# Optimization experiments

Measured on AMD Instinct MI355X. Metric: run time of the kernel, lower is better.

The kernel has to match this reference:

```python
import jax, jax.numpy as jnp
import numpy as np

NUM_CLASSES = 81
NEG_RATIO = 3
POS_FRAC = 0.03  # realistic fraction of positive (matched) anchors


def setup_inputs() -> dict:
    key = jax.random.key(0)
    k1, k2, k3, k4, k5 = jax.random.split(key, 5)
    B, A, C = 64, 8732, NUM_CLASSES
    pred_loc = jax.random.normal(k1, (B, A, 4), dtype=jnp.float32)
    pred_conf = jax.random.normal(k2, (B, A, C), dtype=jnp.float32)
    gt_loc = jax.random.normal(k3, (B, A, 4), dtype=jnp.float32)
    raw_cls = jax.random.randint(k4, (B, A), 1, C)
    is_pos = jax.random.uniform(k5, (B, A)) < POS_FRAC
    gt_label = jnp.where(is_pos, raw_cls, 0).astype(jnp.int32)
    return {"pred_loc": pred_loc, "pred_conf": pred_conf, "gt_loc": gt_loc, "gt_label": gt_label}


def reference(pred_loc, pred_conf, gt_loc, gt_label):
    # pred_loc/gt_loc: [B, A, 4]; pred_conf: [B, A, C]; gt_label: [B, A] int
    pos = gt_label > 0  # [B, A]

    # Smooth L1 (beta=1), summed over positive anchors only (mask instead of boolean gather)
    d = jnp.abs(pred_loc - gt_loc)
    sl1 = jnp.where(d < 1.0, 0.5 * d * d, d - 0.5)
    loc_loss = jnp.sum(sl1 * pos[..., None].astype(sl1.dtype))

    # Per-anchor cross-entropy
    logp = jax.nn.log_softmax(pred_conf, axis=-1)  # [B, A, C]
    ce = -jnp.take_along_axis(logp, gt_label[..., None].astype(jnp.int32), axis=-1)[..., 0]  # [B, A]

    cef = ce.reshape(-1)
    posf = pos.reshape(-1)
    num_pos = jnp.sum(posf)
    num_neg = jnp.minimum(NEG_RATIO * num_pos, posf.size - num_pos)

    # Hard-negative mining: rank negatives by CE descending; select top num_neg.
    neg_vals = jnp.where(posf, -jnp.inf, cef)
    order = jnp.argsort(-neg_vals)  # indices sorted by descending negative loss
    rank = jnp.zeros_like(order).at[order].set(jnp.arange(order.size))
    neg_sel = (rank < num_neg) & (~posf)

    pos_conf_loss = jnp.sum(jnp.where(posf, cef, 0.0))
    neg_conf_loss = jnp.sum(jnp.where(neg_sel, cef, 0.0))

    total = (loc_loss + pos_conf_loss + neg_conf_loss) / num_pos.astype(cef.dtype)
    return total
```

## Files before the change

kernel.cpp:

```cpp
#include <hip/hip_runtime.h>
#include <hip/hip_bf16.h>
#include <math.h>

#define NB   64
#define NA   8732
#define NCLS 81
#define NTOT (NB * NA)
#define NSLICE 64
#define K1BLK  4096
#define SUMBLK 256

#define OFF_KEYS   0
#define OFF_HISTA  (NTOT * 4)
#define OFF_HIST2  (OFF_HISTA + NSLICE * 256 * 4)
#define OFF_SCAL   (OFF_HIST2 + 4096 * 4)
#define OFF_PBNP   (OFF_SCAL + 64)
#define OFF_PBPC   (OFF_PBNP + K1BLK * 4)
#define OFF_PBNEG  (OFF_PBPC + K1BLK * 4)
#define OFF_PBLOC  (OFF_PBNEG + SUMBLK * 4)
#define OFF_PBBIN  (OFF_PBLOC + SUMBLK * 4)
#define ZERO_BYTES (NSLICE * 256 * 4 + 4096 * 4 + 64)

__device__ __forceinline__ unsigned f2k(float f) {
  unsigned u = __float_as_uint(f);
  return (u & 0x80000000u) ? ~u : (u | 0x80000000u);
}
__device__ __forceinline__ float k2fv(unsigned u) {
  return __uint_as_float((u & 0x80000000u) ? (u ^ 0x80000000u) : ~u);
}

#define DPPF(v, ctrl) \
  __int_as_float(__builtin_amdgcn_update_dpp(0, __float_as_int(v), ctrl, 0xF, 0xF, true))

__global__ __launch_bounds__(256, 8) void mbl_k1(
    const float* __restrict__ pred_conf, const int* __restrict__ gt_label,
    unsigned* __restrict__ keys, unsigned* __restrict__ hista,
    unsigned* __restrict__ pb_np, float* __restrict__ pb_pc) {
  __shared__ unsigned lhist[256];
  __shared__ float s_pc[4];
  __shared__ unsigned s_np[4];
  lhist[threadIdx.x] = 0u;
  __syncthreads();

  const int sub = threadIdx.x & 15;
  const int G   = gridDim.x << 4;
  const int base = (blockIdx.x << 4) + (threadIdx.x >> 4);

  float posconf = 0.f;
  unsigned npos = 0u;
  const char* cbase = (const char*)pred_conf;

  float a0, a1, a2, a3, a4, a80; int alab;
  float b0, b1v, b2v, b3, b4, b80; int blab;
  float c0, c1, c2, c3, c4, c80; int clab;

#define LOADS(p0, p1, p2, p3, p4, p80, plab, aa) do {                          \
    const char* _p = cbase + (unsigned)(aa) * 324u + (sub << 2);               \
    p0 = *(const float*)(_p);                                                  \
    p1 = *(const float*)(_p + 64);                                             \
    p2 = *(const float*)(_p + 128);                                            \
    p3 = *(const float*)(_p + 192);                                            \
    p4 = *(const float*)(_p + 256);                                            \
    p80 = (sub == 0) ? *(const float*)(cbase + (unsigned)(aa) * 324u + 320u)   \
                     : 0.f;                                                    \
    plab = gt_label[aa];                                                       \
  } while (0)

#define COMPUTE(p0, p1, p2, p3, p4, p80, plab, aa) do {                        \
    float e = __expf(p0) + __expf(p1) + __expf(p2) + __expf(p3) + __expf(p4);  \
    if (sub == 0) e += __expf(p80);                                            \
    const int _d = (plab) - sub;                                               \
    float pk = (_d == 0)  ? p0 : (_d == 16) ? p1 : (_d == 32) ? p2             \
             : (_d == 48) ? p3 : (_d == 64) ? p4 : (_d == 80) ? p80 : 0.f;     \
    e += DPPF(e, 0xB1);   pk += DPPF(pk, 0xB1);                                \
    e += DPPF(e, 0x4E);   pk += DPPF(pk, 0x4E);                                \
    e += DPPF(e, 0x141);  pk += DPPF(pk, 0x141);                               \
    e += DPPF(e, 0x140);  pk += DPPF(pk, 0x140);                               \
    if (sub == 0) {                                                            \
      const float ce = __logf(e) - pk;                                         \
      if ((plab) > 0) {                                                        \
        npos += 1u; posconf += ce; keys[aa] = 0u;                              \
      } else {                                                                 \
        const unsigned _u = f2k(ce);                                           \
        keys[aa] = _u;                                                         \
        atomicAdd(&lhist[_u >> 24], 1u);                                       \
      }                                                                        \
    }                                                                          \
  } while (0)

  int i0 = base;
  bool v0 = i0 < NTOT;
  if (v0) {
    LOADS(a0, a1, a2, a3, a4, a80, alab, i0);
    int i1 = i0 + G;
    if (i1 < NTOT) LOADS(b0, b1v, b2v, b3, b4, b80, blab, i1);
    int ic = i1 + G;
    for (;;) {
      if (ic < NTOT) LOADS(c0, c1, c2, c3, c4, c80, clab, ic);
      COMPUTE(a0, a1, a2, a3, a4, a80, alab, i0);
      if (!(i1 < NTOT)) break;
      const int in = ic + G;
      if (in < NTOT) LOADS(a0, a1, a2, a3, a4, a80, alab, in);
      COMPUTE(b0, b1v, b2v, b3, b4, b80, blab, i1);
      if (!(ic < NTOT)) break;
      const int in2 = in + G;
      if (in2 < NTOT) LOADS(b0, b1v, b2v, b3, b4, b80, blab, in2);
      COMPUTE(c0, c1, c2, c3, c4, c80, clab, ic);
      if (!(in < NTOT)) break;
      i0 = in; i1 = in2; ic = in2 + G;
    }
  }
#undef LOADS
#undef COMPUTE

#pragma unroll
  for (int s = 1; s < 64; s <<= 1) {
    posconf += __shfl_xor(posconf, s);
    npos    += (unsigned)__shfl_xor((int)npos, s);
  }
  {
    const int wv = threadIdx.x >> 6;
    if ((threadIdx.x & 63) == 0) { s_pc[wv] = posconf; s_np[wv] = npos; }
  }
  __syncthreads();
  if (threadIdx.x == 0) {
    pb_pc[blockIdx.x] = s_pc[0] + s_pc[1] + s_pc[2] + s_pc[3];
    pb_np[blockIdx.x] = s_np[0] + s_np[1] + s_np[2] + s_np[3];
  }
  const unsigned hv = lhist[threadIdx.x];
  if (hv) atomicAdd(&hista[(blockIdx.x & (NSLICE - 1)) * 256 + threadIdx.x], hv);
}

__global__ __launch_bounds__(256) void mbl_sel1(const unsigned* __restrict__ hista,
                                                const unsigned* __restrict__ pb_np,
                                                const float* __restrict__ pb_pc,
                                                unsigned* __restrict__ scal_u,
                                                float* __restrict__ scal_f) {
  __shared__ unsigned partial[256];
  __shared__ float q_pc[4];
  __shared__ unsigned q_np[4];
  __shared__ unsigned s_k;
  const int t = threadIdx.x;

  unsigned np = 0u; float pc = 0.f;
  for (int i = t; i < K1BLK; i += 256) { np += pb_np[i]; pc += pb_pc[i]; }
#pragma unroll
  for (int s = 1; s < 64; s <<= 1) {
    np += (unsigned)__shfl_xor((int)np, s);
    pc += __shfl_xor(pc, s);
  }
  if ((t & 63) == 0) { q_np[t >> 6] = np; q_pc[t >> 6] = pc; }
  __syncthreads();
  if (t == 0) {
    const unsigned tot = q_np[0] + q_np[1] + q_np[2] + q_np[3];
    scal_u[0] = tot;
    scal_f[2] = q_pc[0] + q_pc[1] + q_pc[2] + q_pc[3];
    const unsigned k = min(3u * tot, (unsigned)NTOT - tot);
    s_k = k; scal_u[4] = k;
    if (k == 0u) {
      scal_u[7] = 0xFFFFFFFFu; scal_u[8] = 0u;
      scal_u[9] = 0xFFFFFFFFu; scal_u[10] = 1u;
    }
  }
  __syncthreads();
  const unsigned k = s_k;
  if (k == 0u) return;

  unsigned s = 0u;
  for (int sl = 0; sl < NSLICE; ++sl) s += hista[sl * 256 + t];
  unsigned val = s;
  partial[t] = val;
  __syncthreads();
  for (int off = 1; off < 256; off <<= 1) {
    const unsigned add = (t + off < 256) ? partial[t + off] : 0u;
    __syncthreads();
    val += add;
    partial[t] = val;
    __syncthreads();
  }
  const unsigned suf = val - s;
  if (suf < k && k <= suf + s) { scal_u[5] = (unsigned)t; scal_u[6] = suf; }
}

__global__ __launch_bounds__(256) void mbl_h2(const unsigned* __restrict__ keys,
                                              unsigned* __restrict__ hist2,
                                              const unsigned* __restrict__ scal_u) {
  if (scal_u[4] == 0u) return;
  __shared__ unsigned lh[4096];
  for (int i = threadIdx.x; i < 4096; i += 256) lh[i] = 0u;
  __syncthreads();
  const unsigned b1 = scal_u[5];
  const int stride = gridDim.x * 256;
  for (int i = blockIdx.x * 256 + threadIdx.x; i < NTOT; i += stride) {
    const unsigned key = keys[i];
    if ((key >> 24) == b1) atomicAdd(&lh[(key >> 12) & 0xFFFu], 1u);
  }
  __syncthreads();
  for (int i = threadIdx.x; i < 4096; i += 256) {
    const unsigned v = lh[i];
    if (v) atomicAdd(&hist2[i], v);
  }
}

__global__ __launch_bounds__(1024) void mbl_sel2(const unsigned* __restrict__ hist2,
                                                 unsigned* __restrict__ scal_u) {
  __shared__ unsigned partial[1024];
  if (scal_u[4] == 0u) return;
  const unsigned kt = scal_u[4] - scal_u[6];
  const unsigned b1 = scal_u[5];
  const int t = threadIdx.x;
  unsigned s = 0u;
#pragma unroll
  for (int i = 0; i < 4; ++i) s += hist2[t * 4 + i];
  unsigned val = s;
  partial[t] = val;
  __syncthreads();
  for (int off = 1; off < 1024; off <<= 1) {
    const unsigned add = (t + off < 1024) ? partial[t + off] : 0u;
    __syncthreads();
    val += add;
    partial[t] = val;
    __syncthreads();
  }
  const unsigned suf = val - s;
  if (suf < kt && kt <= suf + s) {
    unsigned c = suf;
    for (int b = 3; b >= 0; --b) {
      const unsigned h = hist2[t * 4 + b];
      if (c + h >= kt) {
        const unsigned bin = (unsigned)(t * 4 + b);
        scal_u[7] = (b1 << 24) | (bin << 12) | 0xFFFu;
        scal_u[9] = (b1 << 12) | bin;
        scal_u[8] = kt - c;
        scal_u[10] = h;
        break;
      }
      c += h;
    }
  }
}

__global__ __launch_bounds__(256) void mbl_sum(
    const unsigned* __restrict__ keys, const int* __restrict__ gt_label,
    const float* __restrict__ pred_loc, const float* __restrict__ gt_loc,
    const unsigned* __restrict__ scal_u,
    float* __restrict__ pb_neg, float* __restrict__ pb_loc,
    float* __restrict__ pb_bin) {
  __shared__ float q_n[4], q_l[4], q_b[4];
  const unsigned T = scal_u[7];
  const unsigned P20 = scal_u[9];
  float acc = 0.f, lacc = 0.f, bacc = 0.f;
  const int stride = gridDim.x * 256;
  for (int i = blockIdx.x * 256 + threadIdx.x; i < NTOT; i += stride) {
    const unsigned key = keys[i];
    if (key > T) acc += k2fv(key);
    else if ((key >> 12) == P20) bacc += k2fv(key);
    const int lb = gt_label[i];
    if (lb > 0) {
      const float4 pl = ((const float4*)pred_loc)[i];
      const float4 gl = ((const float4*)gt_loc)[i];
      float d;
      d = fabsf(pl.x - gl.x); lacc += (d < 1.f) ? 0.5f * d * d : d - 0.5f;
      d = fabsf(pl.y - gl.y); lacc += (d < 1.f) ? 0.5f * d * d : d - 0.5f;
      d = fabsf(pl.z - gl.z); lacc += (d < 1.f) ? 0.5f * d * d : d - 0.5f;
      d = fabsf(pl.w - gl.w); lacc += (d < 1.f) ? 0.5f * d * d : d - 0.5f;
    }
  }
#pragma unroll
  for (int s = 1; s < 64; s <<= 1) {
    acc  += __shfl_xor(acc, s);
    lacc += __shfl_xor(lacc, s);
    bacc += __shfl_xor(bacc, s);
  }
  const int wv = threadIdx.x >> 6;
  if ((threadIdx.x & 63) == 0) { q_n[wv] = acc; q_l[wv] = lacc; q_b[wv] = bacc; }
  __syncthreads();
  if (threadIdx.x == 0) {
    pb_neg[blockIdx.x] = q_n[0] + q_n[1] + q_n[2] + q_n[3];
    pb_loc[blockIdx.x] = q_l[0] + q_l[1] + q_l[2] + q_l[3];
    pb_bin[blockIdx.x] = q_b[0] + q_b[1] + q_b[2] + q_b[3];
  }
}

__global__ __launch_bounds__(256) void mbl_fin(const unsigned* __restrict__ scal_u,
                                               const float* __restrict__ scal_f,
                                               const float* __restrict__ pb_neg,
                                               const float* __restrict__ pb_loc,
                                               const float* __restrict__ pb_bin,
                                               float* __restrict__ out) {
  __shared__ float q_n[4], q_l[4], q_b[4];
  const int t = threadIdx.x;
  float n = pb_neg[t], l = pb_loc[t], b = pb_bin[t];
#pragma unroll
  for (int s = 1; s < 64; s <<= 1) {
    n += __shfl_xor(n, s);
    l += __shfl_xor(l, s);
    b += __shfl_xor(b, s);
  }
  const int wv = t >> 6;
  if ((t & 63) == 0) { q_n[wv] = n; q_l[wv] = l; q_b[wv] = b; }
  __syncthreads();
  if (t == 0) {
    float negsum = q_n[0] + q_n[1] + q_n[2] + q_n[3];
    const float locsum = q_l[0] + q_l[1] + q_l[2] + q_l[3];
    const float binsum = q_b[0] + q_b[1] + q_b[2] + q_b[3];
    const unsigned r = scal_u[8];
    if (r > 0u) negsum += (float)r * (binsum / (float)scal_u[10]);
    out[0] = (locsum + scal_f[2] + negsum) / (float)scal_u[0];
  }
}

extern "C" void kernel_launch(void* const* d_in, const int* in_sizes, int n_in,
                              void* d_out, int out_size, void* d_ws, size_t ws_size,
                              hipStream_t stream) {
  const float* pred_loc  = (const float*)d_in[0];
  const float* pred_conf = (const float*)d_in[1];
  const float* gt_loc    = (const float*)d_in[2];
  const int*   gt_label  = (const int*)d_in[3];
  float* out = (float*)d_out;

  char* ws = (char*)d_ws;
  unsigned* keys   = (unsigned*)(ws + OFF_KEYS);
  unsigned* hista  = (unsigned*)(ws + OFF_HISTA);
  unsigned* hist2  = (unsigned*)(ws + OFF_HIST2);
  unsigned* scal_u = (unsigned*)(ws + OFF_SCAL);
  float*    scal_f = (float*)(ws + OFF_SCAL);
  unsigned* pb_np  = (unsigned*)(ws + OFF_PBNP);
  float*    pb_pc  = (float*)(ws + OFF_PBPC);
  float*    pb_neg = (float*)(ws + OFF_PBNEG);
  float*    pb_loc = (float*)(ws + OFF_PBLOC);
  float*    pb_bin = (float*)(ws + OFF_PBBIN);

  hipMemsetAsync(ws + OFF_HISTA, 0, ZERO_BYTES, stream);

  mbl_k1<<<K1BLK, 256, 0, stream>>>(pred_conf, gt_label, keys, hista, pb_np, pb_pc);
  mbl_sel1<<<1, 256, 0, stream>>>(hista, pb_np, pb_pc, scal_u, scal_f);
  mbl_h2<<<256, 256, 0, stream>>>(keys, hist2, scal_u);
  mbl_sel2<<<1, 1024, 0, stream>>>(hist2, scal_u);
  mbl_sum<<<SUMBLK, 256, 0, stream>>>(keys, gt_label, pred_loc, gt_loc, scal_u,
                                      pb_neg, pb_loc, pb_bin);
  mbl_fin<<<1, 256, 0, stream>>>(scal_u, scal_f, pb_neg, pb_loc, pb_bin, out);
}
```

Baseline: 72.90 us.

## Stage 16-anchor conf tiles through LDS with coalesced float4 loads

The first pass now has each wavefront load a contiguous tile of 16 anchors (16x81 floats) with float4 loads into shared memory. It then computes the softmax denominators from LDS with 4 lanes per anchor, replacing the scalar strided loads and 16-lane DPP reductions. The goal is fully coalesced wide global reads and fewer reduction steps. In exchange it adds LDS traffic, shared-memory footprint, possible bank conflicts, and it drops the three-deep software prefetch pipeline, so latency hiding now depends on occupancy (launch bound lowered to 7).

```diff
diff --git a/kernel.cpp b/kernel.cpp
--- a/kernel.cpp
+++ b/kernel.cpp
@@ -6,6 +6,7 @@
 #define NA   8732
 #define NCLS 81
 #define NTOT (NB * NA)
+#define NTILE (NTOT / 16)
 #define NSLICE 64
 #define K1BLK  4096
 #define SUMBLK 256
@@ -32,96 +33,74 @@
 #define DPPF(v, ctrl) \
   __int_as_float(__builtin_amdgcn_update_dpp(0, __float_as_int(v), ctrl, 0xF, 0xF, true))
 
-__global__ __launch_bounds__(256, 8) void mbl_k1(
+__global__ __launch_bounds__(256, 7) void mbl_k1(
     const float* __restrict__ pred_conf, const int* __restrict__ gt_label,
     unsigned* __restrict__ keys, unsigned* __restrict__ hista,
     unsigned* __restrict__ pb_np, float* __restrict__ pb_pc) {
+  __shared__ float srow[4][1312];
   __shared__ unsigned lhist[256];
   __shared__ float s_pc[4];
   __shared__ unsigned s_np[4];
   lhist[threadIdx.x] = 0u;
   __syncthreads();
 
-  const int sub = threadIdx.x & 15;
-  const int G   = gridDim.x << 4;
-  const int base = (blockIdx.x << 4) + (threadIdx.x >> 4);
+  const int lane = threadIdx.x & 63;
+  const int wid  = threadIdx.x >> 6;
+  const int gw   = (blockIdx.x << 2) + wid;
+  const int l    = lane & 3;
+  const int q    = lane >> 2;
+  float* slice = srow[wid];
+  float4* s4 = (float4*)slice;
 
   float posconf = 0.f;
   unsigned npos = 0u;
-  const char* cbase = (const char*)pred_conf;
-
-  float a0, a1, a2, a3, a4, a80; int alab;
-  float b0, b1v, b2v, b3, b4, b80; int blab;
-  float c0, c1, c2, c3, c4, c80; int clab;
-
-#define LOADS(p0, p1, p2, p3, p4, p80, plab, aa) do {                          \
-    const char* _p = cbase + (unsigned)(aa) * 324u + (sub << 2);               \
-    p0 = *(const float*)(_p);                                                  \
-    p1 = *(const float*)(_p + 64);                                             \
-    p2 = *(const float*)(_p + 128);                                            \
-    p3 = *(const float*)(_p + 192);                                            \
-    p4 = *(const float*)(_p + 256);                                            \
-    p80 = (sub == 0) ? *(const float*)(cbase + (unsigned)(aa) * 324u + 320u)   \
-                     : 0.f;                                                    \
-    plab = gt_label[aa];                                                       \
-  } while (0)
-
-#define COMPUTE(p0, p1, p2, p3, p4, p80, plab, aa) do {                        \
-    float e = __expf(p0) + __expf(p1) + __expf(p2) + __expf(p3) + __expf(p4);  \
-    if (sub == 0) e += __expf(p80);                                            \
-    const int _d = (plab) - sub;                                               \
-    float pk = (_d == 0)  ? p0 : (_d == 16) ? p1 : (_d == 32) ? p2             \
-             : (_d == 48) ? p3 : (_d == 64) ? p4 : (_d == 80) ? p80 : 0.f;     \
-    e += DPPF(e, 0xB1);   pk += DPPF(pk, 0xB1);                                \
-    e += DPPF(e, 0x4E);   pk += DPPF(pk, 0x4E);                                \
-    e += DPPF(e, 0x141);  pk += DPPF(pk, 0x141);                               \
-    e += DPPF(e, 0x140);  pk += DPPF(pk, 0x140);                               \
-    if (sub == 0) {                                                            \
-      const float ce = __logf(e) - pk;                                         \
-      if ((plab) > 0) {                                                        \
-        npos += 1u; posconf += ce; keys[aa] = 0u;                              \
-      } else {                                                                 \
-        const unsigned _u = f2k(ce);                                           \
-        keys[aa] = _u;                                                         \
-        atomicAdd(&lhist[_u >> 24], 1u);                                       \
-      }                                                                        \
-    }                                                                          \
-  } while (0)
-
-  int i0 = base;
-  bool v0 = i0 < NTOT;
-  if (v0) {
-    LOADS(a0, a1, a2, a3, a4, a80, alab, i0);
-    int i1 = i0 + G;
-    if (i1 < NTOT) LOADS(b0, b1v, b2v, b3, b4, b80, blab, i1);
-    int ic = i1 + G;
-    for (;;) {
-      if (ic < NTOT) LOADS(c0, c1, c2, c3, c4, c80, clab, ic);
-      COMPUTE(a0, a1, a2, a3, a4, a80, alab, i0);
-      if (!(i1 < NTOT)) break;
-      const int in = ic + G;
-      if (in < NTOT) LOADS(a0, a1, a2, a3, a4, a80, alab, in);
-      COMPUTE(b0, b1v, b2v, b3, b4, b80, blab, i1);
-      if (!(ic < NTOT)) break;
-      const int in2 = in + G;
-      if (in2 < NTOT) LOADS(b0, b1v, b2v, b3, b4, b80, blab, in2);
-      COMPUTE(c0, c1, c2, c3, c4, c80, clab, ic);
-      if (!(in < NTOT)) break;
-      i0 = in; i1 = in2; ic = in2 + G;
+
+  for (int tile = gw; tile < NTILE; tile += K1BLK * 4) {
+    const float4* src = (const float4*)pred_conf + (unsigned)tile * 324u;
+    const float4 r0 = src[lane];
+    const float4 r1 = src[lane + 64];
+    const float4 r2 = src[lane + 128];
+    const float4 r3 = src[lane + 192];
+    const float4 r4 = src[lane + 256];
+    float4 r5;
+    if (lane < 4) r5 = src[lane + 320];
+    const int lab = gt_label[(tile << 4) + q];
+
+    s4[lane]       = r0;
+    s4[lane + 64]  = r1;
+    s4[lane + 128] = r2;
+    s4[lane + 192] = r3;
+    s4[lane + 256] = r4;
+    if (lane < 4) s4[lane + 320] = r5;
+
+    const int rb = q * 81;
+    float e = 0.f;
+#pragma unroll
+    for (int j = 0; j < 20; ++j) e += __expf(slice[rb + l + 4 * j]);
+    if (l == 0) e += __expf(slice[rb + 80]);
+    e += DPPF(e, 0xB1);
+    e += DPPF(e, 0x4E);
+    const float pick = slice[rb + lab];
+
+    if (l == 0) {
+      const float ce = __logf(e) - pick;
+      const int a = (tile << 4) + q;
+      if (lab > 0) {
+        npos += 1u; posconf += ce; keys[a] = 0u;
+      } else {
+        const unsigned u = f2k(ce);
+        keys[a] = u;
+        atomicAdd(&lhist[u >> 24], 1u);
+      }
     }
   }
-#undef LOADS
-#undef COMPUTE
 
 #pragma unroll
   for (int s = 1; s < 64; s <<= 1) {
     posconf += __shfl_xor(posconf, s);
     npos    += (unsigned)__shfl_xor((int)npos, s);
   }
-  {
-    const int wv = threadIdx.x >> 6;
-    if ((threadIdx.x & 63) == 0) { s_pc[wv] = posconf; s_np[wv] = npos; }
-  }
+  if ((threadIdx.x & 63) == 0) { s_pc[wid] = posconf; s_np[wid] = npos; }
   __syncthreads();
   if (threadIdx.x == 0) {
     pb_pc[blockIdx.x] = s_pc[0] + s_pc[1] + s_pc[2] + s_pc[3];
```

After: 69.98 us. 1.04x faster.
